# Performance work log

Hardware: AMD Instinct MI355X
Metric: run time of the kernel (lower is better)

Reference implementation:

```python
import jax, jax.numpy as jnp
import numpy as np

B, S, D = 32, 4096, 512

def setup_inputs() -> dict:
    key = jax.random.key(0)
    ks = jax.random.split(key, 5)
    scale = 1.0 / np.sqrt(D)
    return {
        "query": jax.random.normal(ks[0], (B, D), jnp.float32),
        "values": jax.random.normal(ks[1], (B, S, D), jnp.float32),
        "W1": jax.random.normal(ks[2], (D, D), jnp.float32) * scale,
        "b1": jnp.zeros((D,), jnp.float32),
        "W2": jax.random.normal(ks[3], (D, D), jnp.float32) * scale,
        "b2": jnp.zeros((D,), jnp.float32),
        "V": jax.random.normal(ks[4], (D, 1), jnp.float32) * scale,
        "bv": jnp.zeros((1,), jnp.float32),
    }

def reference(query, values, W1, b1, W2, b2, V, bv):
    # query: [B, D], values: [B, S, D]
    q_proj = query @ W1 + b1                      # [B, D]
    v_proj = jnp.einsum('bsd,de->bse', values, W2) + b2  # [B, S, D]
    hidden = jnp.tanh(q_proj[:, None, :] + v_proj)       # [B, S, D]
    score = jnp.einsum('bsd,de->bse', hidden, V) + bv    # [B, S, 1]
    attn = jax.nn.softmax(score, axis=1)                 # softmax over seq axis
    context = jnp.sum(attn * values, axis=1)             # [B, D]
    return (context, attn)
```

## Files before the change

kernel.cpp:

```cpp
#include <hip/hip_runtime.h>
#include <hip/hip_bf16.h>
#include <stdint.h>

#define NB 32
#define NS 4096
#define ND 512

typedef __attribute__((ext_vector_type(8))) short short8;
typedef __attribute__((ext_vector_type(4))) float floatx4;
typedef __attribute__((ext_vector_type(2))) float floatx2;
typedef __attribute__((ext_vector_type(4))) unsigned int uint4v;

__device__ __forceinline__ short f2bf(float f) {
    unsigned int u = __builtin_bit_cast(unsigned int, f);
    return (short)((u + 0x8000u) >> 16);
}

__device__ __forceinline__ unsigned int cvt_pk_bf16(float lo, float hi) {
    unsigned int r;
    asm("v_cvt_pk_bf16_f32 %0, %1, %2" : "=v"(r) : "v"(lo), "v"(hi));
    return r;
}

__device__ __forceinline__ float fast_tanh(float x) {
    float e = __expf(2.0f * x);
    return 1.0f - 2.0f * __builtin_amdgcn_rcpf(e + 1.0f);
}

__global__ void __launch_bounds__(256) prep_kernel(
    const float* __restrict__ query, const float* __restrict__ W1,
    const float* __restrict__ b1, const float* __restrict__ b2,
    const float* __restrict__ W2,
    float* __restrict__ qb, unsigned short* __restrict__ W2Tt) {
    const int bx = blockIdx.x;
    const int t  = threadIdx.x;
    if (bx < 256) {
        const int b  = bx >> 3;
        const int es = bx & 7;
        const int col = t & 63, kc = t >> 6;
        __shared__ float q[ND];
        __shared__ float red[256];
        q[t] = query[b * ND + t];
        q[t + 256] = query[b * ND + t + 256];
        __syncthreads();
        float acc = 0.f;
        const float* wp = W1 + (size_t)(kc * 128) * ND + es * 64 + col;
        const float* qp = q + kc * 128;
#pragma unroll 8
        for (int k = 0; k < 128; k++)
            acc += qp[k] * wp[(size_t)k * ND];
        red[t] = acc;
        __syncthreads();
        if (t < 64) {
            float s = red[t] + red[t + 64] + red[t + 128] + red[t + 192];
            int e = es * 64 + t;
            qb[b * ND + e] = s + b1[e] + b2[e];
        }
    } else {
        int g = (bx - 256) * 256 + t;
        int nt = g >> 14;
        int ks = (g >> 10) & 15;
        int kq = (g >> 8) & 3;
        int n  = g & 255;
        int e  = nt * 256 + n;
        int k0 = ks * 32 + kq * 8;
        short8 v;
#pragma unroll
        for (int j = 0; j < 8; j++)
            v[j] = f2bf(W2[(size_t)(k0 + j) * ND + e]);
        *(short8*)&W2Tt[(size_t)g * 8] = v;
    }
}

__global__ void __launch_bounds__(256, 2) scores_kernel(
    const float* __restrict__ values, const unsigned short* __restrict__ W2Tt,
    const float* __restrict__ qb, const float* __restrict__ V,
    float* __restrict__ pscores) {
    const int st = blockIdx.x;
    const int b  = blockIdx.y;
    const int s0 = st * 64;

    __shared__ __align__(16) unsigned short sA[16][2048];
    __shared__ float sQb[ND];
    __shared__ float sV[ND];
    __shared__ float sRed[4][64];

    const int tid  = threadIdx.x;
    const int lane = tid & 63;
    const int wave = tid >> 6;
    const int mr = lane & 15;
    const int q  = lane >> 4;

    sQb[tid] = qb[b * ND + tid];
    sQb[tid + 256] = qb[b * ND + tid + 256];
    sV[tid]  = V[tid];
    sV[tid + 256] = V[tid + 256];

    const int arow = tid >> 2;
    const int ac   = tid & 3;
    const int ardo = arow * 32 + ((ac ^ ((tid >> 3) & 3)) * 8);
    const float* ag = values + ((size_t)b * NS + s0 + arow) * ND + ac * 8;

    {
        floatx4 aq[4][2];
#pragma unroll
        for (int u = 0; u < 4; u++) {
            aq[u][0] = __builtin_nontemporal_load((const floatx4*)(ag + u * 32));
            aq[u][1] = __builtin_nontemporal_load((const floatx4*)(ag + u * 32 + 4));
        }
#pragma unroll
        for (int ks = 0; ks < 16; ks++) {
            const floatx4 a0 = aq[ks & 3][0], a1 = aq[ks & 3][1];
            if (ks < 12) {
                aq[ks & 3][0] = __builtin_nontemporal_load((const floatx4*)(ag + (ks + 4) * 32));
                aq[ks & 3][1] = __builtin_nontemporal_load((const floatx4*)(ag + (ks + 4) * 32 + 4));
            }
            uint4v w;
            w.x = cvt_pk_bf16(a0.x, a0.y); w.y = cvt_pk_bf16(a0.z, a0.w);
            w.z = cvt_pk_bf16(a1.x, a1.y); w.w = cvt_pk_bf16(a1.z, a1.w);
            *(uint4v*)&sA[ks][ardo] = w;
        }
    }
    __syncthreads();

    const int afo = (q ^ ((mr >> 1) & 3)) * 8;
    const unsigned short* bp = W2Tt + (q * 256 + wave * 64 + mr) * 8;

    floatx4 acc[4][4] = {};
    float p[4][4] = {};
    short8 af[2][4], bq[3][4];

#pragma unroll
    for (int i = 0; i < 4; i++)
        af[0][i] = *(const short8*)&sA[0][(i * 16 + mr) * 32 + afo];
#pragma unroll
    for (int j = 0; j < 4; j++)
        bq[0][j] = *(const short8*)(bp + j * 128);
#pragma unroll
    for (int j = 0; j < 4; j++)
        bq[1][j] = *(const short8*)(bp + 8192 + j * 128);

#pragma unroll
    for (int hk = 0; hk < 32; hk++) {
        const int cur = hk & 1, nxt = cur ^ 1;
        const int ks = hk & 15;

        if (hk < 30) {
            const unsigned short* bsrc = bp + (size_t)(hk + 2) * 8192;
#pragma unroll
            for (int j = 0; j < 4; j++)
                bq[(hk + 2) % 3][j] = *(const short8*)(bsrc + j * 128);
        }
        if (hk < 31) {
#pragma unroll
            for (int i = 0; i < 4; i++)
                af[nxt][i] = *(const short8*)&sA[(hk + 1) & 15][(i * 16 + mr) * 32 + afo];
        }

        __builtin_amdgcn_s_setprio(1);
#pragma unroll
        for (int i = 0; i < 4; i++)
#pragma unroll
            for (int j = 0; j < 4; j++)
                acc[i][j] = __builtin_amdgcn_mfma_f32_16x16x32_bf16(af[cur][i], bq[hk % 3][j], acc[i][j], 0, 0, 0);
        __builtin_amdgcn_s_setprio(0);

        if (ks == 15) {
            const int h = hk >> 4;
            float vcoef[4], qadd[4];
#pragma unroll
            for (int j = 0; j < 4; j++) {
                int col = h * 256 + wave * 64 + j * 16 + mr;
                vcoef[j] = sV[col];
                qadd[j]  = sQb[col];
            }
#pragma unroll
            for (int i = 0; i < 4; i++)
#pragma unroll
                for (int r = 0; r < 4; r++) {
                    float s = 0.f;
#pragma unroll
                    for (int j = 0; j < 4; j++)
                        s += fast_tanh(acc[i][j][r] + qadd[j]) * vcoef[j];
                    p[i][r] += s;
                    if (hk < 31) acc[i][0][r] = 0.f;
                }
            if (hk < 31) {
#pragma unroll
                for (int i = 0; i < 4; i++)
#pragma unroll
                    for (int j = 1; j < 4; j++)
                        acc[i][j] = floatx4{0.f, 0.f, 0.f, 0.f};
            }
        }
    }

#pragma unroll
    for (int i = 0; i < 4; i++) {
#pragma unroll
        for (int r = 0; r < 4; r++) {
            float v = p[i][r];
            v += __shfl_xor(v, 1);
            v += __shfl_xor(v, 2);
            v += __shfl_xor(v, 4);
            v += __shfl_xor(v, 8);
            if (mr == 0) sRed[wave][i * 16 + q * 4 + r] = v;
        }
    }
    __syncthreads();
    if (tid < 64) {
        float s = sRed[0][tid] + sRed[1][tid] + sRed[2][tid] + sRed[3][tid];
        pscores[(size_t)b * NS + s0 + tid] = s;
    }
}

__global__ void __launch_bounds__(256) context_softmax_kernel(
    const float* __restrict__ values, const float* __restrict__ pscores,
    float* __restrict__ attn, float* __restrict__ pctx) {
    int sc = blockIdx.x;
    int b  = blockIdx.y;
    int t  = threadIdx.x;
    __shared__ float sAttn[128];
    __shared__ float red[4];
    __shared__ float bcast[2];
    const float* srow = pscores + (size_t)b * NS;
    float v[16];
    float m = -1e30f;
#pragma unroll
    for (int i = 0; i < 16; i++) { v[i] = srow[t + i * 256]; m = fmaxf(m, v[i]); }
    for (int o = 32; o; o >>= 1) m = fmaxf(m, __shfl_xor(m, o));
    if ((t & 63) == 0) red[t >> 6] = m;
    __syncthreads();
    if (t == 0) bcast[0] = fmaxf(fmaxf(red[0], red[1]), fmaxf(red[2], red[3]));
    __syncthreads();
    m = bcast[0];
    float sum = 0.f;
#pragma unroll
    for (int i = 0; i < 16; i++) sum += __expf(v[i] - m);
    for (int o = 32; o; o >>= 1) sum += __shfl_xor(sum, o);
    if ((t & 63) == 0) red[t >> 6] = sum;
    __syncthreads();
    if (t == 0) bcast[1] = red[0] + red[1] + red[2] + red[3];
    __syncthreads();
    float inv = 1.0f / bcast[1];
    if (t < 128) {
        float w = __expf(srow[sc * 128 + t] - m) * inv;
        attn[(size_t)b * NS + sc * 128 + t] = w;
        sAttn[t] = w;
    }
    __syncthreads();
    int d = t * 2;
    const float* vp = values + ((size_t)b * NS + sc * 128) * ND + d;
    float ax = 0.f, ay = 0.f;
#pragma unroll 8
    for (int s = 0; s < 128; s++) {
        float a = sAttn[s];
        floatx2 vv = __builtin_nontemporal_load((const floatx2*)(vp + (size_t)s * ND));
        ax += a * vv.x; ay += a * vv.y;
    }
    pctx[((size_t)sc * 32 + b) * ND + d]     = ax;
    pctx[((size_t)sc * 32 + b) * ND + d + 1] = ay;
}

__global__ void __launch_bounds__(256) context_reduce_kernel(
    const float* __restrict__ pctx, float* __restrict__ ctx) {
    int i = blockIdx.x * 256 + threadIdx.x;
    float s = 0.f;
#pragma unroll
    for (int p = 0; p < 32; p++) s += pctx[(size_t)p * (32 * ND) + i];
    ctx[i] = s;
}

extern "C" void kernel_launch(void* const* d_in, const int* in_sizes, int n_in,
                              void* d_out, int out_size, void* d_ws, size_t ws_size,
                              hipStream_t stream) {
    const float* query  = (const float*)d_in[0];
    const float* values = (const float*)d_in[1];
    const float* W1     = (const float*)d_in[2];
    const float* b1     = (const float*)d_in[3];
    const float* W2     = (const float*)d_in[4];
    const float* b2     = (const float*)d_in[5];
    const float* V      = (const float*)d_in[6];

    float* ctx_out  = (float*)d_out;
    float* attn_out = (float*)d_out + NB * ND;

    char* ws = (char*)d_ws;
    float*          qb      = (float*)ws;
    unsigned short* W2Tt    = (unsigned short*)(ws + (64 << 10));
    float*          pscores = (float*)(ws + (576 << 10));
    float*          pctx    = (float*)(ws + (1088 << 10));

    prep_kernel<<<384, 256, 0, stream>>>(query, W1, b1, b2, W2, qb, W2Tt);
    scores_kernel<<<dim3(64, 32), 256, 0, stream>>>(values, W2Tt, qb, V, pscores);
    context_softmax_kernel<<<dim3(32, 32), 256, 0, stream>>>(values, pscores, attn_out, pctx);
    context_reduce_kernel<<<64, 256, 0, stream>>>(pctx, ctx_out);
}
```

Before: 459.9 us.

## Fuse context accumulation into scores kernel with split online softmax and combine

The scores kernel now computes a per-tile max and exp-sum and accumulates a partial context from the values tile already held in LDS. A small combine kernel then rescales and merges the 64 partials per batch and writes the normalized attention weights. This removes the second full read of the large values tensor and one kernel launch. In exchange, context is now computed from bf16-rounded values rather than fp32, which costs some accuracy, and the combine kernel runs with only 32 blocks.

```diff
diff --git a/kernel.cpp b/kernel.cpp
--- a/kernel.cpp
+++ b/kernel.cpp
@@ -72,10 +72,10 @@
     }
 }
 
-__global__ void __launch_bounds__(256, 2) scores_kernel(
+__global__ void __launch_bounds__(256, 2) scores_ctx_kernel(
     const float* __restrict__ values, const unsigned short* __restrict__ W2Tt,
     const float* __restrict__ qb, const float* __restrict__ V,
-    float* __restrict__ pscores) {
+    float* __restrict__ pscores, float* __restrict__ pctx, float* __restrict__ ml) {
     const int st = blockIdx.x;
     const int b  = blockIdx.y;
     const int s0 = st * 64;
@@ -84,6 +84,7 @@
     __shared__ float sQb[ND];
     __shared__ float sV[ND];
     __shared__ float sRed[4][64];
+    __shared__ float sW[64];
 
     const int tid  = threadIdx.x;
     const int lane = tid & 63;
@@ -209,66 +210,81 @@
     }
     __syncthreads();
     if (tid < 64) {
-        float s = sRed[0][tid] + sRed[1][tid] + sRed[2][tid] + sRed[3][tid];
-        pscores[(size_t)b * NS + s0 + tid] = s;
-    }
-}
-
-__global__ void __launch_bounds__(256) context_softmax_kernel(
-    const float* __restrict__ values, const float* __restrict__ pscores,
-    float* __restrict__ attn, float* __restrict__ pctx) {
-    int sc = blockIdx.x;
-    int b  = blockIdx.y;
-    int t  = threadIdx.x;
-    __shared__ float sAttn[128];
-    __shared__ float red[4];
-    __shared__ float bcast[2];
+        float sv = sRed[0][tid] + sRed[1][tid] + sRed[2][tid] + sRed[3][tid];
+        pscores[(size_t)b * NS + s0 + tid] = sv;
+        float m = sv;
+        for (int o = 32; o; o >>= 1) m = fmaxf(m, __shfl_xor(m, o));
+        float w = __expf(sv - m);
+        float l = w;
+        for (int o = 32; o; o >>= 1) l += __shfl_xor(l, o);
+        sW[tid] = w;
+        if (tid == 0) {
+            int c = b * 64 + st;
+            ml[c * 2]     = m;
+            ml[c * 2 + 1] = l;
+        }
+    }
+    __syncthreads();
+    {
+        const int d0  = tid * 2;
+        const int ks2 = d0 >> 5;
+        const int c2  = (d0 >> 3) & 3;
+        const int j0  = d0 & 7;
+        float cx = 0.f, cy = 0.f;
+#pragma unroll 8
+        for (int row = 0; row < 64; row++) {
+            unsigned int u = *(const unsigned int*)
+                &sA[ks2][row * 32 + ((c2 ^ ((row >> 1) & 3)) * 8) + j0];
+            float w  = sW[row];
+            float vx = __builtin_bit_cast(float, u << 16);
+            float vy = __builtin_bit_cast(float, u & 0xffff0000u);
+            cx += w * vx;
+            cy += w * vy;
+        }
+        floatx2 o; o.x = cx; o.y = cy;
+        *(floatx2*)&pctx[((size_t)st * NB + b) * ND + d0] = o;
+    }
+}
+
+__global__ void __launch_bounds__(256) combine_kernel(
+    const float* __restrict__ pscores, const float* __restrict__ pctx,
+    const float* __restrict__ ml, float* __restrict__ ctx,
+    float* __restrict__ attn) {
+    const int b = blockIdx.x;
+    const int t = threadIdx.x;
+    __shared__ float eF[64];
+    __shared__ float bc[2];
+    if (t < 64) {
+        float m = ml[(b * 64 + t) * 2];
+        float l = ml[(b * 64 + t) * 2 + 1];
+        float M = m;
+        for (int o = 32; o; o >>= 1) M = fmaxf(M, __shfl_xor(M, o));
+        float e  = __expf(m - M);
+        float Lp = l * e;
+        for (int o = 32; o; o >>= 1) Lp += __shfl_xor(Lp, o);
+        eF[t] = e;
+        if (t == 0) { bc[0] = M; bc[1] = 1.0f / Lp; }
+    }
+    __syncthreads();
+    const float M = bc[0], invL = bc[1];
+    {
+        const int d0 = t * 2;
+        float cx = 0.f, cy = 0.f;
+#pragma unroll 8
+        for (int c = 0; c < 64; c++) {
+            floatx2 v = *(const floatx2*)&pctx[((size_t)c * NB + b) * ND + d0];
+            float e = eF[c];
+            cx += e * v.x;
+            cy += e * v.y;
+        }
+        ctx[b * ND + d0]     = cx * invL;
+        ctx[b * ND + d0 + 1] = cy * invL;
+    }
     const float* srow = pscores + (size_t)b * NS;
-    float v[16];
-    float m = -1e30f;
-#pragma unroll
-    for (int i = 0; i < 16; i++) { v[i] = srow[t + i * 256]; m = fmaxf(m, v[i]); }
-    for (int o = 32; o; o >>= 1) m = fmaxf(m, __shfl_xor(m, o));
-    if ((t & 63) == 0) red[t >> 6] = m;
-    __syncthreads();
-    if (t == 0) bcast[0] = fmaxf(fmaxf(red[0], red[1]), fmaxf(red[2], red[3]));
-    __syncthreads();
-    m = bcast[0];
-    float sum = 0.f;
-#pragma unroll
-    for (int i = 0; i < 16; i++) sum += __expf(v[i] - m);
-    for (int o = 32; o; o >>= 1) sum += __shfl_xor(sum, o);
-    if ((t & 63) == 0) red[t >> 6] = sum;
-    __syncthreads();
-    if (t == 0) bcast[1] = red[0] + red[1] + red[2] + red[3];
-    __syncthreads();
-    float inv = 1.0f / bcast[1];
-    if (t < 128) {
-        float w = __expf(srow[sc * 128 + t] - m) * inv;
-        attn[(size_t)b * NS + sc * 128 + t] = w;
-        sAttn[t] = w;
-    }
-    __syncthreads();
-    int d = t * 2;
-    const float* vp = values + ((size_t)b * NS + sc * 128) * ND + d;
-    float ax = 0.f, ay = 0.f;
-#pragma unroll 8
-    for (int s = 0; s < 128; s++) {
-        float a = sAttn[s];
-        floatx2 vv = __builtin_nontemporal_load((const floatx2*)(vp + (size_t)s * ND));
-        ax += a * vv.x; ay += a * vv.y;
-    }
-    pctx[((size_t)sc * 32 + b) * ND + d]     = ax;
-    pctx[((size_t)sc * 32 + b) * ND + d + 1] = ay;
-}
-
-__global__ void __launch_bounds__(256) context_reduce_kernel(
-    const float* __restrict__ pctx, float* __restrict__ ctx) {
-    int i = blockIdx.x * 256 + threadIdx.x;
-    float s = 0.f;
-#pragma unroll
-    for (int p = 0; p < 32; p++) s += pctx[(size_t)p * (32 * ND) + i];
-    ctx[i] = s;
+    float* ao = attn + (size_t)b * NS;
+#pragma unroll
+    for (int i = 0; i < 16; i++)
+        ao[t + i * 256] = __expf(srow[t + i * 256] - M) * invL;
 }
 
 extern "C" void kernel_launch(void* const* d_in, const int* in_sizes, int n_in,
@@ -290,9 +306,9 @@
     unsigned short* W2Tt    = (unsigned short*)(ws + (64 << 10));
     float*          pscores = (float*)(ws + (576 << 10));
     float*          pctx    = (float*)(ws + (1088 << 10));
+    float*          ml      = (float*)(ws + (5184 << 10));
 
     prep_kernel<<<384, 256, 0, stream>>>(query, W1, b1, b2, W2, qb, W2Tt);
-    scores_kernel<<<dim3(64, 32), 256, 0, stream>>>(values, W2Tt, qb, V, pscores);
-    context_softmax_kernel<<<dim3(32, 32), 256, 0, stream>>>(values, pscores, attn_out, pctx);
-    context_reduce_kernel<<<64, 256, 0, stream>>>(pctx, ctx_out);
-}
+    scores_ctx_kernel<<<dim3(64, 32), 256, 0, stream>>>(values, W2Tt, qb, V, pscores, pctx, ml);
+    combine_kernel<<<NB, 256, 0, stream>>>(pscores, pctx, ml, ctx_out, attn_out);
+}
```

New measurement: 429.3 us. 6.6% less time.
